# Optimization experiments

Hardware: AMD Instinct MI355X
Metric: run time of the kernel (lower is better)

Reference implementation:

```python
import jax, jax.numpy as jnp
import numpy as np

B, N, D = 16, 8192, 384   # examples, sentences per example, embedding dim
KN = 16                   # neighbors per node (kNN degree)
K, H, STEPS = 8, 128, 3   # coin dim, hidden dim, walk steps


def setup_inputs() -> dict:
    key = jax.random.key(0)
    ks = jax.random.split(key, 12)
    s = 0.02
    return {
        "sent_embs": jax.random.normal(ks[0], (B, N, D), dtype=jnp.float32),
        "q_embs": jax.random.normal(ks[1], (B, D), dtype=jnp.float32),
        "neighbors": jax.random.randint(ks[2], (B, N, KN), 0, N, dtype=jnp.int32),
        # coin_net: Linear(2D->H), ReLU, Linear(H->K)
        "coin_w1": jax.random.normal(ks[3], (2 * D, H), dtype=jnp.float32) * s,
        "coin_b1": jnp.zeros((H,), dtype=jnp.float32),
        "coin_w2": jax.random.normal(ks[4], (H, K), dtype=jnp.float32) * s,
        "coin_b2": jnp.zeros((K,), dtype=jnp.float32),
        # path_net: Linear(D+K+D->H), ReLU, Linear(H->1)
        "path_w1": jax.random.normal(ks[5], (D + K + D, H), dtype=jnp.float32) * s,
        "path_b1": jnp.zeros((H,), dtype=jnp.float32),
        "path_w2": jax.random.normal(ks[6], (H, 1), dtype=jnp.float32) * s,
        "path_b2": jnp.zeros((1,), dtype=jnp.float32),
    }


def _mlp(x, w1, b1, w2, b2):
    return jax.nn.relu(x @ w1 + b1) @ w2 + b2


def _forward(sent_embs, q_embs, neighbors,
             coin_w1, coin_b1, coin_w2, coin_b2,
             path_w1, path_b1, path_w2, path_b2):
    b, n, d = sent_embs.shape
    k = coin_w2.shape[1]
    q_bcast = jnp.broadcast_to(q_embs[:, None, :], (b, n, d))

    # coin amplitudes per node: [B, N, K]
    amps = _mlp(jnp.concatenate([sent_embs, q_bcast], axis=-1),
                coin_w1, coin_b1, coin_w2, coin_b2)

    # initial uniform walk state: 1/sqrt(N*K)
    state = jnp.full((b, n, k), 1.0 / np.sqrt(n * k), dtype=sent_embs.dtype)

    # adjacency = self-loop + edges row -> neighbors[row]; A @ X == X + masked neighbor gather-sum
    valid = (neighbors >= 0) & (neighbors < n)           # [B, N, KN]
    safe_nbrs = jnp.where(valid, neighbors, 0)
    batch_idx = jnp.arange(b)[:, None, None]

    for _ in range(STEPS):
        ns = state * amps                                # coin step
        gathered = ns[batch_idx, safe_nbrs]              # [B, N, KN, K]
        gathered = jnp.where(valid[..., None], gathered, 0.0)
        ns = ns + gathered.sum(axis=2)                   # sparse.mm(A, ns)
        norm = jnp.linalg.norm(ns.reshape(b, -1), axis=1)[:, None, None]
        state = ns / jnp.where(norm > 0, norm, 1.0)      # renormalize (guard norm==0)

    path_in = jnp.concatenate([sent_embs, state, q_bcast], axis=-1)  # [B, N, D+K+D]
    logits = _mlp(path_in, path_w1, path_b1, path_w2, path_b2)[..., 0]  # [B, N]
    return logits


def reference(sent_embs, q_embs, neighbors,
              coin_w1, coin_b1, coin_w2, coin_b2,
              path_w1, path_b1, path_w2, path_b2):
    return _forward(sent_embs, q_embs, neighbors,
                    coin_w1, coin_b1, coin_w2, coin_b2,
                    path_w1, path_b1, path_w2, path_b2)
```

## Files before the change

### kernel.cpp

```cpp
#include <hip/hip_runtime.h>

#define B_SZ 16
#define N_SZ 8192
#define D_SZ 384
#define KN_SZ 16
#define K_SZ 8
#define H_SZ 128
#define M_TOTAL (B_SZ * N_SZ)
#define KSTEPS 12
#define LDSA_STRIDE 392

typedef short short8 __attribute__((ext_vector_type(8)));
typedef short short4v __attribute__((ext_vector_type(4)));
typedef unsigned short ushort8v __attribute__((ext_vector_type(8)));
typedef float floatx4 __attribute__((ext_vector_type(4)));

__device__ __forceinline__ unsigned short f2bf(float f) {
    unsigned u = __builtin_bit_cast(unsigned, f);
    u += 0x7FFFu + ((u >> 16) & 1u);
    return (unsigned short)(u >> 16);
}
__device__ __forceinline__ float bf2f(unsigned short b) {
    unsigned u = ((unsigned)b) << 16;
    return __builtin_bit_cast(float, u);
}

__global__ void prep_wswz(const float* __restrict__ coin_w1,
                          const float* __restrict__ path_w1,
                          unsigned short* __restrict__ wswz) {
    int f = blockIdx.x * 256 + threadIdx.x;
    int j  = f & 7;
    int l  = (f >> 3) & 63;
    int ss = (f >> 9) % KSTEPS;
    int ct = f / (KSTEPS * 512);
    int k = ss * 32 + ((l >> 4) << 3) + j;
    int n = ct * 16 + (l & 15);
    float v = (n < H_SZ) ? coin_w1[k * H_SZ + n]
                         : path_w1[k * H_SZ + (n - H_SZ)];
    wswz[f] = f2bf(v);
}

__global__ void prep_q(const float* __restrict__ q_embs,
                       const float* __restrict__ coin_w1,
                       const float* __restrict__ coin_b1,
                       const float* __restrict__ path_w1,
                       const float* __restrict__ path_b1,
                       float* __restrict__ qcoin, float* __restrict__ qpath) {
    int b = blockIdx.x;
    int t = threadIdx.x;
    const float* q = q_embs + b * D_SZ;
    if (t < H_SZ) {
        float acc = coin_b1[t];
        for (int d = 0; d < D_SZ; d++)
            acc += q[d] * coin_w1[(D_SZ + d) * H_SZ + t];
        qcoin[b * H_SZ + t] = acc;
    } else {
        int h = t - H_SZ;
        float acc = path_b1[h];
        for (int d = 0; d < D_SZ; d++)
            acc += q[d] * path_w1[(D_SZ + K_SZ + d) * H_SZ + h];
        qpath[b * H_SZ + h] = acc;
    }
}

__global__ __launch_bounds__(256, 2)
void gemm_fused(const float* __restrict__ sent,
                const unsigned short* __restrict__ wswz,
                unsigned short* __restrict__ hcoin,
                unsigned short* __restrict__ hpath) {
    __shared__ short als[16 * LDSA_STRIDE];
    const int tid = threadIdx.x;
    const int wave = tid >> 6, lane = tid & 63;
    const int m_lane = lane & 15, quad = lane >> 4;

    short8 bfrag[4][KSTEPS];
#pragma unroll
    for (int c = 0; c < 4; c++) {
        int ct = wave * 4 + c;
#pragma unroll
        for (int s = 0; s < KSTEPS; s++) {
            bfrag[c][s] = *(const short8*)(wswz + ((((ct * KSTEPS + s) * 64) + lane) << 3));
        }
    }

    for (int mt = blockIdx.x; mt < M_TOTAL / 16; mt += gridDim.x) {
        const float* abase = sent + (size_t)mt * 16 * D_SZ;
#pragma unroll
        for (int i = 0; i < 6; i++) {
            int e4 = i * 256 + tid;
            int row = e4 / 96;
            int c4  = e4 - row * 96;
            float4 v = *(const float4*)(abase + (size_t)e4 * 4);
            short4v sv;
            sv.x = (short)f2bf(v.x); sv.y = (short)f2bf(v.y);
            sv.z = (short)f2bf(v.z); sv.w = (short)f2bf(v.w);
            *(short4v*)&als[row * LDSA_STRIDE + c4 * 4] = sv;
        }
        __syncthreads();

        floatx4 acc[4];
#pragma unroll
        for (int c = 0; c < 4; c++) acc[c] = (floatx4){0.f, 0.f, 0.f, 0.f};

#pragma unroll
        for (int s = 0; s < KSTEPS; s++) {
            short8 afrag = *(const short8*)&als[m_lane * LDSA_STRIDE + s * 32 + quad * 8];
#pragma unroll
            for (int c = 0; c < 4; c++)
                acc[c] = __builtin_amdgcn_mfma_f32_16x16x32_bf16(afrag, bfrag[c][s], acc[c], 0, 0, 0);
        }
        __syncthreads();

        unsigned short* dstbase = (wave < 2) ? hcoin : hpath;
        int colbase = (wave & 1) * 64;
#pragma unroll
        for (int c = 0; c < 4; c++) {
            int col = colbase + c * 16 + m_lane;
#pragma unroll
            for (int r = 0; r < 4; r++) {
                int rowg = mt * 16 + quad * 4 + r;
                dstbase[(size_t)rowg * H_SZ + col] = f2bf(acc[c][r]);
            }
        }
    }
}

__global__ __launch_bounds__(256)
void amps_kernel(const unsigned short* __restrict__ hcoin,
                 const float* __restrict__ qcoin,
                 const float* __restrict__ coin_w2,
                 const float* __restrict__ coin_b2,
                 float* __restrict__ amps) {
    __shared__ float w2s[H_SZ * K_SZ];
    __shared__ float qcs[H_SZ];
    const int tid = threadIdx.x;
    const int m = blockIdx.x * 256 + tid;
    const int b = m >> 13;
    for (int i = tid; i < H_SZ * K_SZ; i += 256) w2s[i] = coin_w2[i];
    if (tid < H_SZ) qcs[tid] = qcoin[b * H_SZ + tid];
    __syncthreads();

    float acc[K_SZ];
#pragma unroll
    for (int j = 0; j < K_SZ; j++) acc[j] = coin_b2[j];

    const unsigned short* hrow = hcoin + (size_t)m * H_SZ;
    for (int h0 = 0; h0 < H_SZ; h0 += 8) {
        ushort8v hv8 = *(const ushort8v*)(hrow + h0);
#pragma unroll
        for (int t = 0; t < 8; t++) {
            float hv = bf2f(hv8[t]) + qcs[h0 + t];
            hv = hv > 0.f ? hv : 0.f;
#pragma unroll
            for (int j = 0; j < K_SZ; j++) acc[j] += hv * w2s[(h0 + t) * K_SZ + j];
        }
    }
    float4 o0 = {acc[0], acc[1], acc[2], acc[3]};
    float4 o1 = {acc[4], acc[5], acc[6], acc[7]};
    *(float4*)(amps + (size_t)m * 8)     = o0;
    *(float4*)(amps + (size_t)m * 8 + 4) = o1;
}

__global__ void walk_init(const float* __restrict__ amps,
                          float* __restrict__ nsA, float* __restrict__ norms) {
    int idx = blockIdx.x * 256 + threadIdx.x;
    const float c0 = 1.0f / 256.0f;
    float4 v = ((const float4*)amps)[idx];
    v.x *= c0; v.y *= c0; v.z *= c0; v.w *= c0;
    ((float4*)nsA)[idx] = v;
    if (blockIdx.x == 0 && threadIdx.x < 48) norms[threadIdx.x] = 0.f;
}

__global__ __launch_bounds__(256)
void walk_gather(const float* __restrict__ ns,
                 const int* __restrict__ neighbors,
                 float* __restrict__ outns,
                 float* __restrict__ norms, int step) {
    const int m = blockIdx.x * 256 + threadIdx.x;
    const int b = m >> 13;
    const size_t nbase = (size_t)b << 13;

    float v[K_SZ];
    {
        float4 a0 = *(const float4*)(ns + (size_t)m * 8);
        float4 a1 = *(const float4*)(ns + (size_t)m * 8 + 4);
        v[0] = a0.x; v[1] = a0.y; v[2] = a0.z; v[3] = a0.w;
        v[4] = a1.x; v[5] = a1.y; v[6] = a1.z; v[7] = a1.w;
    }
    const int4* nb4 = (const int4*)(neighbors + (size_t)m * KN_SZ);
    int nbr[KN_SZ];
#pragma unroll
    for (int i = 0; i < 4; i++) *(int4*)&nbr[i * 4] = nb4[i];
#pragma unroll
    for (int i = 0; i < KN_SZ; i++) {
        int nn = nbr[i];
        if (nn >= 0 && nn < N_SZ) {
            const float* p = ns + (nbase + nn) * 8;
            float4 g0 = *(const float4*)p;
            float4 g1 = *(const float4*)(p + 4);
            v[0] += g0.x; v[1] += g0.y; v[2] += g0.z; v[3] += g0.w;
            v[4] += g1.x; v[5] += g1.y; v[6] += g1.z; v[7] += g1.w;
        }
    }
    float4 o0 = {v[0], v[1], v[2], v[3]};
    float4 o1 = {v[4], v[5], v[6], v[7]};
    *(float4*)(outns + (size_t)m * 8)     = o0;
    *(float4*)(outns + (size_t)m * 8 + 4) = o1;

    float ss = 0.f;
#pragma unroll
    for (int j = 0; j < K_SZ; j++) ss += v[j] * v[j];
#pragma unroll
    for (int off = 32; off > 0; off >>= 1) ss += __shfl_down(ss, off);

    __shared__ float blocksum;
    if (threadIdx.x == 0) blocksum = 0.f;
    __syncthreads();
    if ((threadIdx.x & 63) == 0) atomicAdd(&blocksum, ss);
    __syncthreads();
    if (threadIdx.x == 0) atomicAdd(&norms[step * B_SZ + b], blocksum);
}

__global__ void walk_scale_coin(const float* __restrict__ inns,
                                const float* __restrict__ amps,
                                const float* __restrict__ norms, int prevstep,
                                float* __restrict__ outns) {
    int idx = blockIdx.x * 256 + threadIdx.x;
    int b = idx >> 14;
    float ssq = norms[prevstep * B_SZ + b];
    float inv = ssq > 0.f ? rsqrtf(ssq) : 1.0f;
    float4 vv = ((const float4*)inns)[idx];
    float4 aa = ((const float4*)amps)[idx];
    vv.x *= inv * aa.x; vv.y *= inv * aa.y; vv.z *= inv * aa.z; vv.w *= inv * aa.w;
    ((float4*)outns)[idx] = vv;
}

__global__ __launch_bounds__(256)
void logits_kernel(const unsigned short* __restrict__ hpath,
                   const float* __restrict__ qpath,
                   const float* __restrict__ nsB,
                   const float* __restrict__ norms,
                   const float* __restrict__ path_w1,
                   const float* __restrict__ path_w2,
                   const float* __restrict__ path_b2,
                   float* __restrict__ out) {
    __shared__ float w1s[K_SZ * H_SZ];
    __shared__ float w2s[H_SZ];
    __shared__ float qps[H_SZ];
    const int tid = threadIdx.x;
    const int m = blockIdx.x * 256 + tid;
    const int b = m >> 13;
    for (int i = tid; i < K_SZ * H_SZ; i += 256) w1s[i] = path_w1[D_SZ * H_SZ + i];
    if (tid < H_SZ) { w2s[tid] = path_w2[tid]; qps[tid] = qpath[b * H_SZ + tid]; }
    __syncthreads();

    float ssq = norms[2 * B_SZ + b];
    float inv = ssq > 0.f ? rsqrtf(ssq) : 1.0f;
    float st[K_SZ];
    {
        float4 s0 = *(const float4*)(nsB + (size_t)m * 8);
        float4 s1 = *(const float4*)(nsB + (size_t)m * 8 + 4);
        st[0] = s0.x * inv; st[1] = s0.y * inv; st[2] = s0.z * inv; st[3] = s0.w * inv;
        st[4] = s1.x * inv; st[5] = s1.y * inv; st[6] = s1.z * inv; st[7] = s1.w * inv;
    }

    float acc = path_b2[0];
    const unsigned short* hrow = hpath + (size_t)m * H_SZ;
    for (int h0 = 0; h0 < H_SZ; h0 += 8) {
        ushort8v hv8 = *(const ushort8v*)(hrow + h0);
#pragma unroll
        for (int t = 0; t < 8; t++) {
            int h = h0 + t;
            float hv = bf2f(hv8[t]) + qps[h];
#pragma unroll
            for (int j = 0; j < K_SZ; j++) hv += st[j] * w1s[j * H_SZ + h];
            hv = hv > 0.f ? hv : 0.f;
            acc += hv * w2s[h];
        }
    }
    out[m] = acc;
}

extern "C" void kernel_launch(void* const* d_in, const int* in_sizes, int n_in,
                              void* d_out, int out_size, void* d_ws, size_t ws_size,
                              hipStream_t stream) {
    const float* sent      = (const float*)d_in[0];
    const float* q_embs    = (const float*)d_in[1];
    const int*   neighbors = (const int*)d_in[2];
    const float* coin_w1   = (const float*)d_in[3];
    const float* coin_b1   = (const float*)d_in[4];
    const float* coin_w2   = (const float*)d_in[5];
    const float* coin_b2   = (const float*)d_in[6];
    const float* path_w1   = (const float*)d_in[7];
    const float* path_b1   = (const float*)d_in[8];
    const float* path_w2   = (const float*)d_in[9];
    const float* path_b2   = (const float*)d_in[10];
    float* out = (float*)d_out;

    char* ws = (char*)d_ws;
    unsigned short* wswz = (unsigned short*)ws;
    float* qcoin = (float*)(ws + 196608);
    float* qpath = (float*)(ws + 196608 + 8192);
    float* norms = (float*)(ws + 196608 + 16384);
    unsigned short* hcoin = (unsigned short*)(ws + 213248);
    unsigned short* hpath = hcoin + (size_t)M_TOTAL * H_SZ;
    float* amps = (float*)(ws + 213248 + 2ull * 33554432ull);
    float* nsA  = amps + (size_t)M_TOTAL * K_SZ;
    float* nsB  = nsA  + (size_t)M_TOTAL * K_SZ;

    prep_wswz<<<384, 256, 0, stream>>>(coin_w1, path_w1, wswz);
    prep_q<<<B_SZ, 256, 0, stream>>>(q_embs, coin_w1, coin_b1, path_w1, path_b1, qcoin, qpath);
    gemm_fused<<<2048, 256, 0, stream>>>(sent, wswz, hcoin, hpath);
    amps_kernel<<<M_TOTAL / 256, 256, 0, stream>>>(hcoin, qcoin, coin_w2, coin_b2, amps);

    walk_init<<<1024, 256, 0, stream>>>(amps, nsA, norms);
    walk_gather<<<M_TOTAL / 256, 256, 0, stream>>>(nsA, neighbors, nsB, norms, 0);
    walk_scale_coin<<<1024, 256, 0, stream>>>(nsB, amps, norms, 0, nsA);
    walk_gather<<<M_TOTAL / 256, 256, 0, stream>>>(nsA, neighbors, nsB, norms, 1);
    walk_scale_coin<<<1024, 256, 0, stream>>>(nsB, amps, norms, 1, nsA);
    walk_gather<<<M_TOTAL / 256, 256, 0, stream>>>(nsA, neighbors, nsB, norms, 2);
    logits_kernel<<<M_TOTAL / 256, 256, 0, stream>>>(hpath, qpath, nsB, norms, path_w1, path_w2, path_b2, out);
}
```

Measured before the change: 435.8 us.

## Defer walk normalization, fuse walk kernels, block hidden layout, merge prep kernels

Normalization is scale-invariant, so the intermediate per-step renormalizations are dropped and only the final norm is computed. The coin multiply is fused into the gather step, and walk_init is folded into the amps kernel, removing several launches and full-array passes. The GEMM now processes 64-row tiles per block and stores hidden activations in a 16-row blocked layout, so the consumer kernels read them with coalesced loads. The walk gather splits each node across two threads. The prep kernels are merged into one launch. Skipping intermediate normalization risks overflow or underflow if the amplitudes grow or shrink a lot over the steps.

```diff
diff --git a/kernel.cpp b/kernel.cpp
--- a/kernel.cpp
+++ b/kernel.cpp
@@ -9,10 +9,11 @@
 #define M_TOTAL (B_SZ * N_SZ)
 #define KSTEPS 12
 #define LDSA_STRIDE 392
+#define MT64 (M_TOTAL / 64)
+#define GEMM_GRID 512
 
 typedef short short8 __attribute__((ext_vector_type(8)));
 typedef short short4v __attribute__((ext_vector_type(4)));
-typedef unsigned short ushort8v __attribute__((ext_vector_type(8)));
 typedef float floatx4 __attribute__((ext_vector_type(4)));
 
 __device__ __forceinline__ unsigned short f2bf(float f) {
@@ -25,50 +26,53 @@
     return __builtin_bit_cast(float, u);
 }
 
-__global__ void prep_wswz(const float* __restrict__ coin_w1,
-                          const float* __restrict__ path_w1,
-                          unsigned short* __restrict__ wswz) {
-    int f = blockIdx.x * 256 + threadIdx.x;
-    int j  = f & 7;
-    int l  = (f >> 3) & 63;
-    int ss = (f >> 9) % KSTEPS;
-    int ct = f / (KSTEPS * 512);
-    int k = ss * 32 + ((l >> 4) << 3) + j;
-    int n = ct * 16 + (l & 15);
-    float v = (n < H_SZ) ? coin_w1[k * H_SZ + n]
-                         : path_w1[k * H_SZ + (n - H_SZ)];
-    wswz[f] = f2bf(v);
-}
-
-__global__ void prep_q(const float* __restrict__ q_embs,
-                       const float* __restrict__ coin_w1,
-                       const float* __restrict__ coin_b1,
-                       const float* __restrict__ path_w1,
-                       const float* __restrict__ path_b1,
-                       float* __restrict__ qcoin, float* __restrict__ qpath) {
-    int b = blockIdx.x;
+__global__ void prep_kernel(const float* __restrict__ q_embs,
+                            const float* __restrict__ coin_w1,
+                            const float* __restrict__ coin_b1,
+                            const float* __restrict__ path_w1,
+                            const float* __restrict__ path_b1,
+                            unsigned short* __restrict__ wswz,
+                            float* __restrict__ qcoin, float* __restrict__ qpath,
+                            float* __restrict__ norms) {
+    int blk = blockIdx.x;
     int t = threadIdx.x;
-    const float* q = q_embs + b * D_SZ;
-    if (t < H_SZ) {
-        float acc = coin_b1[t];
-        for (int d = 0; d < D_SZ; d++)
-            acc += q[d] * coin_w1[(D_SZ + d) * H_SZ + t];
-        qcoin[b * H_SZ + t] = acc;
+    if (blk < 384) {
+        int f = blk * 256 + t;
+        int j  = f & 7;
+        int l  = (f >> 3) & 63;
+        int ss = (f >> 9) % KSTEPS;
+        int ct = f / (KSTEPS * 512);
+        int k = ss * 32 + ((l >> 4) << 3) + j;
+        int n = ct * 16 + (l & 15);
+        float v = (n < H_SZ) ? coin_w1[k * H_SZ + n]
+                             : path_w1[k * H_SZ + (n - H_SZ)];
+        wswz[f] = f2bf(v);
+    } else if (blk == 384) {
+        if (t < B_SZ) norms[t] = 0.f;
     } else {
-        int h = t - H_SZ;
-        float acc = path_b1[h];
-        for (int d = 0; d < D_SZ; d++)
-            acc += q[d] * path_w1[(D_SZ + K_SZ + d) * H_SZ + h];
-        qpath[b * H_SZ + h] = acc;
+        int b = blk - 385;
+        const float* q = q_embs + b * D_SZ;
+        if (t < H_SZ) {
+            float acc = coin_b1[t];
+            for (int d = 0; d < D_SZ; d++)
+                acc += q[d] * coin_w1[(D_SZ + d) * H_SZ + t];
+            qcoin[b * H_SZ + t] = acc;
+        } else if (t < 2 * H_SZ) {
+            int h = t - H_SZ;
+            float acc = path_b1[h];
+            for (int d = 0; d < D_SZ; d++)
+                acc += q[d] * path_w1[(D_SZ + K_SZ + d) * H_SZ + h];
+            qpath[b * H_SZ + h] = acc;
+        }
     }
 }
 
 __global__ __launch_bounds__(256, 2)
 void gemm_fused(const float* __restrict__ sent,
                 const unsigned short* __restrict__ wswz,
-                unsigned short* __restrict__ hcoin,
-                unsigned short* __restrict__ hpath) {
-    __shared__ short als[16 * LDSA_STRIDE];
+                unsigned short* __restrict__ hcoinB,
+                unsigned short* __restrict__ hpathB) {
+    __shared__ short als[64 * LDSA_STRIDE];
     const int tid = threadIdx.x;
     const int wave = tid >> 6, lane = tid & 63;
     const int m_lane = lane & 15, quad = lane >> 4;
@@ -78,205 +82,183 @@
     for (int c = 0; c < 4; c++) {
         int ct = wave * 4 + c;
 #pragma unroll
-        for (int s = 0; s < KSTEPS; s++) {
+        for (int s = 0; s < KSTEPS; s++)
             bfrag[c][s] = *(const short8*)(wswz + ((((ct * KSTEPS + s) * 64) + lane) << 3));
-        }
-    }
-
-    for (int mt = blockIdx.x; mt < M_TOTAL / 16; mt += gridDim.x) {
-        const float* abase = sent + (size_t)mt * 16 * D_SZ;
-#pragma unroll
-        for (int i = 0; i < 6; i++) {
-            int e4 = i * 256 + tid;
-            int row = e4 / 96;
-            int c4  = e4 - row * 96;
-            float4 v = *(const float4*)(abase + (size_t)e4 * 4);
-            short4v sv;
-            sv.x = (short)f2bf(v.x); sv.y = (short)f2bf(v.y);
-            sv.z = (short)f2bf(v.z); sv.w = (short)f2bf(v.w);
-            *(short4v*)&als[row * LDSA_STRIDE + c4 * 4] = sv;
+    }
+
+    unsigned short* dstbase = (wave < 2) ? hcoinB : hpathB;
+    const int colw = (wave & 1) * 64;
+
+    for (int mt = blockIdx.x; mt < MT64; mt += GEMM_GRID) {
+        const float* abase = sent + (size_t)mt * 64 * D_SZ;
+#pragma unroll
+        for (int cc = 0; cc < 6; cc++) {
+            float4 v[4];
+#pragma unroll
+            for (int u = 0; u < 4; u++)
+                v[u] = *(const float4*)(abase + (size_t)((cc * 4 + u) * 256 + tid) * 4);
+#pragma unroll
+            for (int u = 0; u < 4; u++) {
+                int e4 = (cc * 4 + u) * 256 + tid;
+                int row = e4 / 96;
+                int c4  = e4 - row * 96;
+                short4v sv;
+                sv.x = (short)f2bf(v[u].x); sv.y = (short)f2bf(v[u].y);
+                sv.z = (short)f2bf(v[u].z); sv.w = (short)f2bf(v[u].w);
+                *(short4v*)&als[row * LDSA_STRIDE + c4 * 4] = sv;
+            }
         }
         __syncthreads();
 
-        floatx4 acc[4];
-#pragma unroll
-        for (int c = 0; c < 4; c++) acc[c] = (floatx4){0.f, 0.f, 0.f, 0.f};
-
-#pragma unroll
-        for (int s = 0; s < KSTEPS; s++) {
-            short8 afrag = *(const short8*)&als[m_lane * LDSA_STRIDE + s * 32 + quad * 8];
-#pragma unroll
-            for (int c = 0; c < 4; c++)
-                acc[c] = __builtin_amdgcn_mfma_f32_16x16x32_bf16(afrag, bfrag[c][s], acc[c], 0, 0, 0);
+        for (int rt = 0; rt < 4; rt++) {
+            floatx4 acc[4];
+#pragma unroll
+            for (int c = 0; c < 4; c++) acc[c] = (floatx4){0.f, 0.f, 0.f, 0.f};
+#pragma unroll
+            for (int s = 0; s < KSTEPS; s++) {
+                short8 afrag = *(const short8*)&als[(rt * 16 + m_lane) * LDSA_STRIDE + s * 32 + quad * 8];
+#pragma unroll
+                for (int c = 0; c < 4; c++)
+                    acc[c] = __builtin_amdgcn_mfma_f32_16x16x32_bf16(afrag, bfrag[c][s], acc[c], 0, 0, 0);
+            }
+            int mt16 = mt * 4 + rt;
+#pragma unroll
+            for (int c = 0; c < 4; c++) {
+                int col = colw + c * 16 + m_lane;
+                short4v sv;
+                sv.x = (short)f2bf(acc[c][0]); sv.y = (short)f2bf(acc[c][1]);
+                sv.z = (short)f2bf(acc[c][2]); sv.w = (short)f2bf(acc[c][3]);
+                *(short4v*)(dstbase + (size_t)mt16 * 2048 + col * 16 + quad * 4) = sv;
+            }
         }
         __syncthreads();
-
-        unsigned short* dstbase = (wave < 2) ? hcoin : hpath;
-        int colbase = (wave & 1) * 64;
-#pragma unroll
-        for (int c = 0; c < 4; c++) {
-            int col = colbase + c * 16 + m_lane;
-#pragma unroll
-            for (int r = 0; r < 4; r++) {
-                int rowg = mt * 16 + quad * 4 + r;
-                dstbase[(size_t)rowg * H_SZ + col] = f2bf(acc[c][r]);
-            }
-        }
     }
 }
 
 __global__ __launch_bounds__(256)
-void amps_kernel(const unsigned short* __restrict__ hcoin,
-                 const float* __restrict__ qcoin,
-                 const float* __restrict__ coin_w2,
-                 const float* __restrict__ coin_b2,
-                 float* __restrict__ amps) {
+void amps_init_kernel(const unsigned short* __restrict__ hcoinB,
+                      const float* __restrict__ qcoin,
+                      const float* __restrict__ coin_w2,
+                      const float* __restrict__ coin_b2,
+                      float* __restrict__ amps, float* __restrict__ z0) {
     __shared__ float w2s[H_SZ * K_SZ];
     __shared__ float qcs[H_SZ];
     const int tid = threadIdx.x;
     const int m = blockIdx.x * 256 + tid;
-    const int b = m >> 13;
+    const int b = (blockIdx.x * 256) >> 13;
     for (int i = tid; i < H_SZ * K_SZ; i += 256) w2s[i] = coin_w2[i];
     if (tid < H_SZ) qcs[tid] = qcoin[b * H_SZ + tid];
     __syncthreads();
 
+    const unsigned short* hb = hcoinB + (size_t)(m >> 4) * 2048 + (m & 15);
     float acc[K_SZ];
 #pragma unroll
     for (int j = 0; j < K_SZ; j++) acc[j] = coin_b2[j];
 
-    const unsigned short* hrow = hcoin + (size_t)m * H_SZ;
-    for (int h0 = 0; h0 < H_SZ; h0 += 8) {
-        ushort8v hv8 = *(const ushort8v*)(hrow + h0);
-#pragma unroll
-        for (int t = 0; t < 8; t++) {
-            float hv = bf2f(hv8[t]) + qcs[h0 + t];
-            hv = hv > 0.f ? hv : 0.f;
-#pragma unroll
-            for (int j = 0; j < K_SZ; j++) acc[j] += hv * w2s[(h0 + t) * K_SZ + j];
-        }
-    }
+    for (int h = 0; h < H_SZ; h++) {
+        float hv = bf2f(hb[h * 16]) + qcs[h];
+        hv = hv > 0.f ? hv : 0.f;
+        float4 wa = *(const float4*)&w2s[h * 8];
+        float4 wb = *(const float4*)&w2s[h * 8 + 4];
+        acc[0] += hv * wa.x; acc[1] += hv * wa.y; acc[2] += hv * wa.z; acc[3] += hv * wa.w;
+        acc[4] += hv * wb.x; acc[5] += hv * wb.y; acc[6] += hv * wb.z; acc[7] += hv * wb.w;
+    }
+    const float c0 = 1.0f / 256.0f;
     float4 o0 = {acc[0], acc[1], acc[2], acc[3]};
     float4 o1 = {acc[4], acc[5], acc[6], acc[7]};
     *(float4*)(amps + (size_t)m * 8)     = o0;
     *(float4*)(amps + (size_t)m * 8 + 4) = o1;
-}
-
-__global__ void walk_init(const float* __restrict__ amps,
-                          float* __restrict__ nsA, float* __restrict__ norms) {
-    int idx = blockIdx.x * 256 + threadIdx.x;
-    const float c0 = 1.0f / 256.0f;
-    float4 v = ((const float4*)amps)[idx];
-    v.x *= c0; v.y *= c0; v.z *= c0; v.w *= c0;
-    ((float4*)nsA)[idx] = v;
-    if (blockIdx.x == 0 && threadIdx.x < 48) norms[threadIdx.x] = 0.f;
+    float4 s0 = {acc[0]*c0, acc[1]*c0, acc[2]*c0, acc[3]*c0};
+    float4 s1 = {acc[4]*c0, acc[5]*c0, acc[6]*c0, acc[7]*c0};
+    *(float4*)(z0 + (size_t)m * 8)     = s0;
+    *(float4*)(z0 + (size_t)m * 8 + 4) = s1;
 }
 
 __global__ __launch_bounds__(256)
-void walk_gather(const float* __restrict__ ns,
-                 const int* __restrict__ neighbors,
-                 float* __restrict__ outns,
-                 float* __restrict__ norms, int step) {
-    const int m = blockIdx.x * 256 + threadIdx.x;
+void walk_step(const float* __restrict__ z,
+               const int* __restrict__ neighbors,
+               const float* __restrict__ amps,
+               float* __restrict__ outz,
+               float* __restrict__ norms, int last) {
+    const int g = blockIdx.x * 256 + threadIdx.x;
+    const int m = g >> 1, half = g & 1;
     const int b = m >> 13;
     const size_t nbase = (size_t)b << 13;
-
-    float v[K_SZ];
-    {
-        float4 a0 = *(const float4*)(ns + (size_t)m * 8);
-        float4 a1 = *(const float4*)(ns + (size_t)m * 8 + 4);
-        v[0] = a0.x; v[1] = a0.y; v[2] = a0.z; v[3] = a0.w;
-        v[4] = a1.x; v[5] = a1.y; v[6] = a1.z; v[7] = a1.w;
-    }
+    const int off = half * 4;
+
+    float4 v = *(const float4*)(z + (size_t)m * 8 + off);
+    int nbr[KN_SZ];
     const int4* nb4 = (const int4*)(neighbors + (size_t)m * KN_SZ);
-    int nbr[KN_SZ];
 #pragma unroll
     for (int i = 0; i < 4; i++) *(int4*)&nbr[i * 4] = nb4[i];
 #pragma unroll
     for (int i = 0; i < KN_SZ; i++) {
         int nn = nbr[i];
         if (nn >= 0 && nn < N_SZ) {
-            const float* p = ns + (nbase + nn) * 8;
-            float4 g0 = *(const float4*)p;
-            float4 g1 = *(const float4*)(p + 4);
-            v[0] += g0.x; v[1] += g0.y; v[2] += g0.z; v[3] += g0.w;
-            v[4] += g1.x; v[5] += g1.y; v[6] += g1.z; v[7] += g1.w;
+            float4 gv = *(const float4*)(z + (nbase + nn) * 8 + off);
+            v.x += gv.x; v.y += gv.y; v.z += gv.z; v.w += gv.w;
         }
     }
-    float4 o0 = {v[0], v[1], v[2], v[3]};
-    float4 o1 = {v[4], v[5], v[6], v[7]};
-    *(float4*)(outns + (size_t)m * 8)     = o0;
-    *(float4*)(outns + (size_t)m * 8 + 4) = o1;
-
-    float ss = 0.f;
-#pragma unroll
-    for (int j = 0; j < K_SZ; j++) ss += v[j] * v[j];
-#pragma unroll
-    for (int off = 32; off > 0; off >>= 1) ss += __shfl_down(ss, off);
-
-    __shared__ float blocksum;
-    if (threadIdx.x == 0) blocksum = 0.f;
-    __syncthreads();
-    if ((threadIdx.x & 63) == 0) atomicAdd(&blocksum, ss);
-    __syncthreads();
-    if (threadIdx.x == 0) atomicAdd(&norms[step * B_SZ + b], blocksum);
-}
-
-__global__ void walk_scale_coin(const float* __restrict__ inns,
-                                const float* __restrict__ amps,
-                                const float* __restrict__ norms, int prevstep,
-                                float* __restrict__ outns) {
-    int idx = blockIdx.x * 256 + threadIdx.x;
-    int b = idx >> 14;
-    float ssq = norms[prevstep * B_SZ + b];
-    float inv = ssq > 0.f ? rsqrtf(ssq) : 1.0f;
-    float4 vv = ((const float4*)inns)[idx];
-    float4 aa = ((const float4*)amps)[idx];
-    vv.x *= inv * aa.x; vv.y *= inv * aa.y; vv.z *= inv * aa.z; vv.w *= inv * aa.w;
-    ((float4*)outns)[idx] = vv;
+    if (!last) {
+        float4 a = *(const float4*)(amps + (size_t)m * 8 + off);
+        v.x *= a.x; v.y *= a.y; v.z *= a.z; v.w *= a.w;
+        *(float4*)(outz + (size_t)m * 8 + off) = v;
+    } else {
+        *(float4*)(outz + (size_t)m * 8 + off) = v;
+        float ss = v.x * v.x + v.y * v.y + v.z * v.z + v.w * v.w;
+#pragma unroll
+        for (int o = 32; o > 0; o >>= 1) ss += __shfl_down(ss, o);
+        __shared__ float blocksum;
+        if (threadIdx.x == 0) blocksum = 0.f;
+        __syncthreads();
+        if ((threadIdx.x & 63) == 0) atomicAdd(&blocksum, ss);
+        __syncthreads();
+        if (threadIdx.x == 0) atomicAdd(&norms[b], blocksum);
+    }
 }
 
 __global__ __launch_bounds__(256)
-void logits_kernel(const unsigned short* __restrict__ hpath,
+void logits_kernel(const unsigned short* __restrict__ hpathB,
                    const float* __restrict__ qpath,
-                   const float* __restrict__ nsB,
+                   const float* __restrict__ u2,
                    const float* __restrict__ norms,
                    const float* __restrict__ path_w1,
                    const float* __restrict__ path_w2,
                    const float* __restrict__ path_b2,
                    float* __restrict__ out) {
-    __shared__ float w1s[K_SZ * H_SZ];
+    __shared__ float w1t[H_SZ * K_SZ];
     __shared__ float w2s[H_SZ];
     __shared__ float qps[H_SZ];
     const int tid = threadIdx.x;
     const int m = blockIdx.x * 256 + tid;
-    const int b = m >> 13;
-    for (int i = tid; i < K_SZ * H_SZ; i += 256) w1s[i] = path_w1[D_SZ * H_SZ + i];
+    const int b = (blockIdx.x * 256) >> 13;
+    for (int i = tid; i < H_SZ * K_SZ; i += 256) {
+        int h = i >> 3, j = i & 7;
+        w1t[i] = path_w1[(D_SZ + j) * H_SZ + h];
+    }
     if (tid < H_SZ) { w2s[tid] = path_w2[tid]; qps[tid] = qpath[b * H_SZ + tid]; }
     __syncthreads();
 
-    float ssq = norms[2 * B_SZ + b];
+    float ssq = norms[b];
     float inv = ssq > 0.f ? rsqrtf(ssq) : 1.0f;
     float st[K_SZ];
     {
-        float4 s0 = *(const float4*)(nsB + (size_t)m * 8);
-        float4 s1 = *(const float4*)(nsB + (size_t)m * 8 + 4);
+        float4 s0 = *(const float4*)(u2 + (size_t)m * 8);
+        float4 s1 = *(const float4*)(u2 + (size_t)m * 8 + 4);
         st[0] = s0.x * inv; st[1] = s0.y * inv; st[2] = s0.z * inv; st[3] = s0.w * inv;
         st[4] = s1.x * inv; st[5] = s1.y * inv; st[6] = s1.z * inv; st[7] = s1.w * inv;
     }
 
+    const unsigned short* hb = hpathB + (size_t)(m >> 4) * 2048 + (m & 15);
     float acc = path_b2[0];
-    const unsigned short* hrow = hpath + (size_t)m * H_SZ;
-    for (int h0 = 0; h0 < H_SZ; h0 += 8) {
-        ushort8v hv8 = *(const ushort8v*)(hrow + h0);
-#pragma unroll
-        for (int t = 0; t < 8; t++) {
-            int h = h0 + t;
-            float hv = bf2f(hv8[t]) + qps[h];
-#pragma unroll
-            for (int j = 0; j < K_SZ; j++) hv += st[j] * w1s[j * H_SZ + h];
-            hv = hv > 0.f ? hv : 0.f;
-            acc += hv * w2s[h];
-        }
+    for (int h = 0; h < H_SZ; h++) {
+        float hv = bf2f(hb[h * 16]) + qps[h];
+        float4 wa = *(const float4*)&w1t[h * 8];
+        float4 wb = *(const float4*)&w1t[h * 8 + 4];
+        hv += st[0]*wa.x + st[1]*wa.y + st[2]*wa.z + st[3]*wa.w
+            + st[4]*wb.x + st[5]*wb.y + st[6]*wb.z + st[7]*wb.w;
+        hv = hv > 0.f ? hv : 0.f;
+        acc += hv * w2s[h];
     }
     out[m] = acc;
 }
@@ -302,22 +284,19 @@
     float* qcoin = (float*)(ws + 196608);
     float* qpath = (float*)(ws + 196608 + 8192);
     float* norms = (float*)(ws + 196608 + 16384);
-    unsigned short* hcoin = (unsigned short*)(ws + 213248);
-    unsigned short* hpath = hcoin + (size_t)M_TOTAL * H_SZ;
+    unsigned short* hcoinB = (unsigned short*)(ws + 213248);
+    unsigned short* hpathB = hcoinB + (size_t)M_TOTAL * H_SZ;
     float* amps = (float*)(ws + 213248 + 2ull * 33554432ull);
-    float* nsA  = amps + (size_t)M_TOTAL * K_SZ;
-    float* nsB  = nsA  + (size_t)M_TOTAL * K_SZ;
-
-    prep_wswz<<<384, 256, 0, stream>>>(coin_w1, path_w1, wswz);
-    prep_q<<<B_SZ, 256, 0, stream>>>(q_embs, coin_w1, coin_b1, path_w1, path_b1, qcoin, qpath);
-    gemm_fused<<<2048, 256, 0, stream>>>(sent, wswz, hcoin, hpath);
-    amps_kernel<<<M_TOTAL / 256, 256, 0, stream>>>(hcoin, qcoin, coin_w2, coin_b2, amps);
-
-    walk_init<<<1024, 256, 0, stream>>>(amps, nsA, norms);
-    walk_gather<<<M_TOTAL / 256, 256, 0, stream>>>(nsA, neighbors, nsB, norms, 0);
-    walk_scale_coin<<<1024, 256, 0, stream>>>(nsB, amps, norms, 0, nsA);
-    walk_gather<<<M_TOTAL / 256, 256, 0, stream>>>(nsA, neighbors, nsB, norms, 1);
-    walk_scale_coin<<<1024, 256, 0, stream>>>(nsB, amps, norms, 1, nsA);
-    walk_gather<<<M_TOTAL / 256, 256, 0, stream>>>(nsA, neighbors, nsB, norms, 2);
-    logits_kernel<<<M_TOTAL / 256, 256, 0, stream>>>(hpath, qpath, nsB, norms, path_w1, path_w2, path_b2, out);
-}
+    float* zA   = amps + (size_t)M_TOTAL * K_SZ;
+    float* zB   = zA   + (size_t)M_TOTAL * K_SZ;
+
+    prep_kernel<<<401, 256, 0, stream>>>(q_embs, coin_w1, coin_b1, path_w1, path_b1,
+                                         wswz, qcoin, qpath, norms);
+    gemm_fused<<<GEMM_GRID, 256, 0, stream>>>(sent, wswz, hcoinB, hpathB);
+    amps_init_kernel<<<M_TOTAL / 256, 256, 0, stream>>>(hcoinB, qcoin, coin_w2, coin_b2, amps, zA);
+    walk_step<<<2 * M_TOTAL / 256, 256, 0, stream>>>(zA, neighbors, amps, zB, norms, 0);
+    walk_step<<<2 * M_TOTAL / 256, 256, 0, stream>>>(zB, neighbors, amps, zA, norms, 0);
+    walk_step<<<2 * M_TOTAL / 256, 256, 0, stream>>>(zA, neighbors, amps, zB, norms, 1);
+    logits_kernel<<<M_TOTAL / 256, 256, 0, stream>>>(hpathB, qpath, zB, norms,
+                                                     path_w1, path_w2, path_b2, out);
+}
```

New measurement: 421.7 us. -3.2%, faster.
